# Optimization experiments

Measured on AMD Instinct MI355X. Metric: run time of the kernel, lower is better.

Reference implementation:

```python
import jax, jax.numpy as jnp
import numpy as np
from jax import lax

DN = ('NCHW', 'OIHW', 'NCHW')


def conv3x3(x, w, b):
    y = lax.conv_general_dilated(x, w, (1, 1), [(1, 1), (1, 1)], dimension_numbers=DN)
    return y + b[None, :, None, None]


def lrelu(x, s):
    return jnp.where(x >= 0, x, s * x)


def layernorm_c(x, g, b, eps=1e-5):
    # LayerNorm over embed_dim; tokens are (h,w), so normalize the channel axis
    m = jnp.mean(x, axis=1, keepdims=True)
    v = jnp.var(x, axis=1, keepdims=True)
    return (x - m) / jnp.sqrt(v + eps) * g[None, :, None, None] + b[None, :, None, None]


def bilateral_corr(x1, x2, md):
    # bilateral cost volume on L2-normalized features:
    # out[b,d,h,w] = <x1n[b,:,h-dy,w-dx], x2n[b,:,h+dy,w+dx]>, (dy,dx) in [-md,md]^2
    def l2n(x):
        return x / jnp.maximum(jnp.linalg.norm(x, axis=1, keepdims=True), 1e-12)
    x1n, x2n = l2n(x1), l2n(x2)
    B, C, H, W = x1.shape
    p1 = jnp.pad(x1n, ((0, 0), (0, 0), (md, md), (md, md)))
    p2 = jnp.pad(x2n, ((0, 0), (0, 0), (md, md), (md, md)))
    outs = []
    for dy in range(-md, md + 1):
        for dx in range(-md, md + 1):
            a = p1[:, :, md - dy:md - dy + H, md - dx:md - dx + W]
            b = p2[:, :, md + dy:md + dy + H, md + dx:md + dx + W]
            outs.append(jnp.sum(a * b, axis=1))
    return jnp.stack(outs, axis=1)  # [B, (2md+1)^2, H, W]


def tail(xt, bi, gln, bln, w0, b0, wr1, br1, wr2, br2, w2, b2, w3, b3, wdec, bdec, wf, bf):
    xt = layernorm_c(xt, gln, bln)
    y = conv3x3(jnp.concatenate([xt, bi], axis=1), w0, b0)
    # resblock(64,64): lrelu(conv2(lrelu(conv1(y))) + y), slope 0.1
    s = y
    r = lrelu(conv3x3(y, wr1, br1), 0.1)
    r = conv3x3(r, wr2, br2) + s
    y = lrelu(r, 0.1)
    y = lrelu(conv3x3(y, w2, b2), 0.2)
    y = lrelu(conv3x3(y, w3, b3), 0.2)
    # ConvTranspose2d(64,64,3,stride=2,pad=1,out_pad=1): lhs-dilated conv with flipped kernel
    wd = jnp.transpose(jnp.flip(wdec, (-2, -1)), (1, 0, 2, 3))  # torch [in,out,kh,kw] -> OIHW
    y = lax.conv_general_dilated(y, wd, (1, 1), [(1, 2), (1, 2)], lhs_dilation=(2, 2), dimension_numbers=DN) + bdec[None, :, None, None]
    flow = conv3x3(y, wf, bf)  # [B, 2, 2H, 2W]
    B, _, H2, W2 = flow.shape
    # F.interpolate(scale_factor=4, mode='bilinear', align_corners=False) * 4
    return jax.image.resize(flow, (B, 2, 4 * H2, 4 * W2), method='bilinear') * 4.0


def setup_inputs():
    key = jax.random.key(0)
    ks = jax.random.split(key, 16)
    B, C, H, W = 4, 256, 96, 160
    md = 3
    r = lambda k, s, sc=0.05: jax.random.normal(k, s, jnp.float32) * sc
    return {
        'x1': jax.random.normal(ks[0], (B, C, H, W), jnp.float32),
        'x2': jax.random.normal(ks[1], (B, C, H, W), jnp.float32),
        'xt': jax.random.normal(ks[2], (B, C, H, W), jnp.float32),
        'gln': jnp.ones((C,), jnp.float32),
        'bln': jnp.zeros((C,), jnp.float32),
        'w0': r(ks[3], (64, C + (2 * md + 1) ** 2, 3, 3)),
        'b0': jnp.zeros((64,), jnp.float32),
        'wr1': r(ks[4], (64, 64, 3, 3)), 'br1': jnp.zeros((64,), jnp.float32),
        'wr2': r(ks[5], (64, 64, 3, 3)), 'br2': jnp.zeros((64,), jnp.float32),
        'w2': r(ks[6], (64, 64, 3, 3)), 'b2': jnp.zeros((64,), jnp.float32),
        'w3': r(ks[7], (64, 64, 3, 3)), 'b3': jnp.zeros((64,), jnp.float32),
        'wdec': r(ks[8], (64, 64, 3, 3)), 'bdec': jnp.zeros((64,), jnp.float32),
        'wf': r(ks[9], (2, 64, 3, 3)), 'bf': jnp.zeros((2,), jnp.float32),
        'corr_range': 3,
    }


def reference(x1, x2, xt, gln, bln, w0, b0, wr1, br1, wr2, br2, w2, b2, w3, b3, wdec, bdec, wf, bf, corr_range):
    bi = bilateral_corr(x1, x2, int(corr_range))
    return tail(xt, bi, gln, bln, w0, b0, wr1, br1, wr2, br2, w2, b2, w3, b3, wdec, bdec, wf, bf)
```

## Files before the change

kernel.cpp:

```cpp
#include <hip/hip_runtime.h>
#include <math.h>

#define HH_ 96
#define WW_ 160
#define HW 15360
#define NPIX 61440
#define CC 256
#define C0 320
#define FF 64
#define H2 192
#define W2 320
#define OHW 61440
#define HO 768
#define WO 1280

typedef __attribute__((ext_vector_type(8))) short short8;
typedef __attribute__((ext_vector_type(4))) float f32x4;

__device__ __forceinline__ float bf2f(ushort u) {
    union { unsigned int i; float f; } v; v.i = ((unsigned int)u) << 16; return v.f;
}
__device__ __forceinline__ ushort f2bf(float f) {
    union { float f; unsigned int i; } v; v.f = f;
    unsigned int u = v.i;
    return (ushort)((u + 0x7FFFu + ((u >> 16) & 1u)) >> 16);
}

__global__ __launch_bounds__(256) void normpack_kernel(
    const float* __restrict__ x1, const float* __restrict__ x2, const float* __restrict__ xt,
    const float* __restrict__ gam, const float* __restrict__ bet,
    ushort* __restrict__ x1c, ushort* __restrict__ x2c,
    ushort* __restrict__ Xhi, float* __restrict__ inv1, float* __restrict__ inv2) {
    __shared__ ushort tile[32 * 258];
    __shared__ float sred[4][32][2];
    const int t = threadIdx.x;
    const int w = t >> 6, l = t & 63;
    const int px4 = l & 7;
    const int cbase = t >> 3;
    const int pxt = blockIdx.x, which = blockIdx.y, b = blockIdx.z;
    const float* src = (which == 0 ? x1 : which == 1 ? x2 : xt);
    src += (size_t)b * CC * HW + pxt * 32;

    float s1[4] = {0.f, 0.f, 0.f, 0.f}, s2[4] = {0.f, 0.f, 0.f, 0.f};
#pragma unroll
    for (int it = 0; it < 8; ++it) {
        int c = it * 32 + cbase;
        f32x4 v4 = *(const f32x4*)(src + (size_t)c * HW + px4 * 4);
#pragma unroll
        for (int j = 0; j < 4; ++j) {
            float f = v4[j];
            s1[j] += f; s2[j] += f * f;
            tile[(px4 * 4 + j) * 258 + c] = f2bf(f);
        }
    }
#pragma unroll
    for (int j = 0; j < 4; ++j) {
        s1[j] += __shfl_xor(s1[j], 8);  s1[j] += __shfl_xor(s1[j], 16); s1[j] += __shfl_xor(s1[j], 32);
        s2[j] += __shfl_xor(s2[j], 8);  s2[j] += __shfl_xor(s2[j], 16); s2[j] += __shfl_xor(s2[j], 32);
    }
    if ((l >> 3) == 0) {
#pragma unroll
        for (int j = 0; j < 4; ++j) {
            sred[w][px4 * 4 + j][0] = s1[j];
            sred[w][px4 * 4 + j][1] = s2[j];
        }
    }
    __syncthreads();

    const int px = t >> 3, grp = t & 7;
    float S1 = sred[0][px][0] + sred[1][px][0] + sred[2][px][0] + sred[3][px][0];
    float S2 = sred[0][px][1] + sred[1][px][1] + sred[2][px][1] + sred[3][px][1];
    const int p = b * HW + pxt * 32 + px;
    const ushort* row = &tile[px * 258];
    if (which < 2) {
        float inv = 1.f / fmaxf(sqrtf(S2), 1e-12f);
        if (grp == 0) (which == 0 ? inv1 : inv2)[p] = inv;
        ushort* dst = (which == 0 ? x1c : x2c) + (size_t)p * CC + grp * 32;
#pragma unroll
        for (int k = 0; k < 4; ++k) {
            short8 o;
#pragma unroll
            for (int h = 0; h < 4; ++h) {
                unsigned int u2 = *(const unsigned int*)(row + grp * 32 + k * 8 + h * 2);
                o[h * 2]     = (short)(u2 & 0xFFFF);
                o[h * 2 + 1] = (short)(u2 >> 16);
            }
            *(short8*)(dst + k * 8) = o;
        }
    } else {
        float m = S1 * (1.f / 256.f);
        float var = fmaxf(S2 * (1.f / 256.f) - m * m, 0.f);
        float rs = rsqrtf(var + 1e-5f);
        ushort* dst = Xhi + (size_t)p * C0 + grp * 32;
#pragma unroll
        for (int k = 0; k < 4; ++k) {
            short8 o;
#pragma unroll
            for (int h = 0; h < 4; ++h) {
                unsigned int u2 = *(const unsigned int*)(row + grp * 32 + k * 8 + h * 2);
                int c = grp * 32 + k * 8 + h * 2;
                float f0 = (bf2f((ushort)(u2 & 0xFFFF)) - m) * rs * gam[c] + bet[c];
                float f1 = (bf2f((ushort)(u2 >> 16)) - m) * rs * gam[c + 1] + bet[c + 1];
                o[h * 2]     = (short)f2bf(f0);
                o[h * 2 + 1] = (short)f2bf(f1);
            }
            *(short8*)(dst + k * 8) = o;
        }
        if (grp < 4) {
            short8 z = {0, 0, 0, 0, 0, 0, 0, 0};
            *(short8*)(Xhi + (size_t)p * C0 + 256 + grp * 16) = z;
            *(short8*)(Xhi + (size_t)p * C0 + 256 + grp * 16 + 8) = z;
        }
    }
}

__global__ __launch_bounds__(256) void corr_mfma_kernel(
    const ushort* __restrict__ x1c, const ushort* __restrict__ x2c,
    const float* __restrict__ inv1, const float* __restrict__ inv2,
    ushort* __restrict__ Xhi) {
    const int lane = threadIdx.x & 63;
    const int wv = threadIdx.x >> 6;
    const int sid = ((blockIdx.x & 7) * 120) + (blockIdx.x >> 3);
    const int b  = sid / 240;
    const int rem = sid % 240;
    const int uq = rem / 10, xt = rem % 10;
    const int u = uq * 4 + wv;
    const int x0 = xt * 16;
    const int jl = lane & 15;
    const int kg = lane >> 4;
    const short8 zero8 = {0, 0, 0, 0, 0, 0, 0, 0};

    short8 qf[8];
    {
        size_t qb = ((size_t)b * HW + u * WW_ + x0 + jl) * CC + kg * 8;
#pragma unroll
        for (int ks = 0; ks < 8; ++ks)
            qf[ks] = *(const short8*)(x1c + qb + ks * 32);
    }
    float iv1v[4];
#pragma unroll
    for (int r = 0; r < 4; ++r)
        iv1v[r] = inv1[b * HW + u * WW_ + x0 + kg * 4 + r];

    for (int dy = -3; dy <= 3; ++dy) {
        const int y = u + dy;
        if ((unsigned)y >= (unsigned)HH_) continue;
        const int w = u + 2 * dy;
        const bool rowok = (unsigned)w < (unsigned)HH_;

        f32x4 acc0 = (f32x4){0.f, 0.f, 0.f, 0.f};
        f32x4 acc1 = (f32x4){0.f, 0.f, 0.f, 0.f};
        if (rowok) {
#pragma unroll
            for (int nt = 0; nt < 2; ++nt) {
                int kx = x0 - 6 + jl + 16 * nt;
                bool ok = (unsigned)kx < (unsigned)WW_;
                int kxc = min(max(kx, 0), WW_ - 1);
                size_t kb = ((size_t)b * HW + w * WW_ + kxc) * CC + kg * 8;
#pragma unroll
                for (int ks = 0; ks < 8; ++ks) {
                    short8 bv = *(const short8*)(x2c + kb + ks * 32);
                    if (!ok) bv = zero8;
                    if (nt == 0)
                        acc0 = __builtin_amdgcn_mfma_f32_16x16x32_bf16(qf[ks], bv, acc0, 0, 0, 0);
                    else
                        acc1 = __builtin_amdgcn_mfma_f32_16x16x32_bf16(qf[ks], bv, acc1, 0, 0, 0);
                }
            }
        }
#pragma unroll
        for (int nt = 0; nt < 2; ++nt) {
            int j = jl + 16 * nt;
#pragma unroll
            for (int r = 0; r < 4; ++r) {
                int q = kg * 4 + r;
                int tt = j - q - 6;
                if (tt & 1) continue;
                int dx = tt >> 1;
                if (dx < -3 || dx > 3) continue;
                int cx = x0 + q + dx;
                if ((unsigned)cx >= (unsigned)WW_) continue;
                float v = 0.f;
                if (rowok) {
                    int pbx = min(max(x0 + q + 2 * dx, 0), WW_ - 1);
                    float iv2 = inv2[b * HW + w * WW_ + pbx];
                    v = (nt == 0 ? acc0[r] : acc1[r]) * iv1v[r] * iv2;
                }
                size_t o = ((size_t)(b * HW + y * WW_ + cx)) * C0
                         + 256 + (dy + 3) * 7 + (dx + 3);
                Xhi[o] = f2bf(v);
            }
        }
    }
}

__global__ void pack_w_all(const float* __restrict__ w0, const float* __restrict__ wr1,
                           const float* __restrict__ wr2, const float* __restrict__ w2,
                           const float* __restrict__ w3, const float* __restrict__ wdec,
                           ushort* __restrict__ W0, ushort* __restrict__ WR1,
                           ushort* __restrict__ WR2, ushort* __restrict__ W2o,
                           ushort* __restrict__ W3o, ushort* __restrict__ WD) {
    int job = blockIdx.y;
    const float* w = job == 0 ? w0 : job == 1 ? wr1 : job == 2 ? wr2
                   : job == 3 ? w2 : job == 4 ? w3 : wdec;
    ushort* dst = job == 0 ? W0 : job == 1 ? WR1 : job == 2 ? WR2
                : job == 3 ? W2o : job == 4 ? W3o : WD;
    int CinReal = job == 0 ? 305 : 64;
    int KC = job == 0 ? 10 : 2;
    int isDeconv = (job == 5);
    int gid = blockIdx.x * blockDim.x + threadIdx.x;
    int total = 9 * KC * 4 * 64;
    if (gid >= total) return;
    int lane = gid & 63;
    int nt = (gid >> 6) & 3;
    int kc = (gid >> 8) % KC;
    int slot = (gid >> 8) / KC;
    int co = nt * 16 + (lane & 15);
    int ky = slot / 3, kx = slot % 3;
    for (int j = 0; j < 8; ++j) {
        int ci = kc * 32 + (lane >> 4) * 8 + j;
        float v = 0.f;
        if (ci < CinReal) {
            if (isDeconv) v = w[((size_t)(ci * 64 + co) * 3 + (2 - ky)) * 3 + (2 - kx)];
            else          v = w[((size_t)(co * CinReal + ci) * 3 + ky) * 3 + kx];
        }
        dst[(size_t)gid * 8 + j] = f2bf(v);
    }
}

template<int KC>
__global__ __launch_bounds__(256, 8) void conv_ldsK(
    const ushort* __restrict__ Ahi,
    const ushort* __restrict__ Whi,
    const float* __restrict__ bias,
    ushort* __restrict__ Ohi,
    const ushort* __restrict__ Rhi,
    float slope, int act, int hasres) {
    constexpr int CIN = KC * 32;
    __shared__ ushort lds[2 * 2336];
    const int t = threadIdx.x;
    const int lane = t & 63;
    const int wave = t >> 6;
    const int row_w = wave >> 1;
    const int coh = wave & 1;
    const int kg = lane >> 4;
    const int jl = lane & 15;
    const short8 zero8 = {0, 0, 0, 0, 0, 0, 0, 0};

    const int sid = ((blockIdx.x & 7) * 240) + (blockIdx.x >> 3);
    const int b0 = sid / 480;
    const int rm = sid % 480;
    const int yp = rm / 10, xw = rm % 10;
    const int y0 = yp * 2;
    const int x0 = xw * 16;
    const size_t rowbase = (size_t)b0 * HW;

    f32x4 acc[2];
    acc[0] = (f32x4){0.f, 0.f, 0.f, 0.f};
    acc[1] = (f32x4){0.f, 0.f, 0.f, 0.f};

    auto stage = [&](ushort* buf, int kc) {
#pragma unroll
        for (int i = 0; i < 2; ++i) {
            int e = t + i * 256;
            if (e < 288) {
                int kge = e & 3;
                int q = e >> 2;
                int pe = q % 18;
                int re = q / 18;
                int gy = y0 - 1 + re, gx = x0 - 1 + pe;
                bool ok = ((unsigned)gy < 96u) && ((unsigned)gx < 160u);
                short8 vh = zero8;
                if (ok) {
                    size_t ga = ((rowbase + gy * WW_ + gx) * (size_t)CIN) + kc * 32 + kge * 8;
                    vh = *(const short8*)(Ahi + ga);
                }
                *(short8*)(buf + kge * 584 + (re * 18 + pe) * 8) = vh;
            }
        }
    };

    stage(lds, 0);

#pragma unroll 1
    for (int kc = 0; kc < KC; ++kc) {
        __syncthreads();
        if (kc + 1 < KC) stage(lds + ((kc + 1) & 1) * 2336, kc + 1);
        const ushort* bufc = lds + (kc & 1) * 2336;
#pragma unroll
        for (int tap = 0; tap < 9; ++tap) {
            const int dy = tap / 3 - 1, dx = tap % 3 - 1;
            const int abase = kg * 584 + (row_w + dy + 1) * 144 + (jl + dx + 1) * 8;
            short8 ah = *(const short8*)(bufc + abase);
            const ushort* wt = Whi + (size_t)(tap * KC + kc) * 2048;
#pragma unroll
            for (int nt = 0; nt < 2; ++nt) {
                short8 bh = *(const short8*)(wt + (((coh << 1) | nt) * 64 + lane) * 8);
                acc[nt] = __builtin_amdgcn_mfma_f32_16x16x32_bf16(ah, bh, acc[nt], 0, 0, 0);
            }
        }
    }

#pragma unroll
    for (int r = 0; r < 4; ++r) {
        size_t pr = rowbase + (y0 + row_w) * WW_ + x0 + kg * 4 + r;
#pragma unroll
        for (int nt = 0; nt < 2; ++nt) {
            int co = ((coh << 1) | nt) * 16 + jl;
            float vv = acc[nt][r] + bias[co];
            size_t oo = pr * 64 + co;
            if (hasres) vv += bf2f(Rhi[oo]);
            if (act) vv = vv >= 0.f ? vv : vv * slope;
            Ohi[oo] = f2bf(vv);
        }
    }
}

__global__ __launch_bounds__(256, 6) void deconv_fused_kernel(
    const ushort* __restrict__ Ahi,
    const ushort* __restrict__ Whi,
    const float* __restrict__ bias,
    ushort* __restrict__ decb) {
    const int lane = threadIdx.x & 63;
    const int wave = threadIdx.x >> 6;
    const int row_w = wave >> 1;
    const int coh = wave & 1;
    const int kg = lane >> 4;
    const short8 zero8 = {0, 0, 0, 0, 0, 0, 0, 0};

    const int sid = ((blockIdx.x & 7) * 240) + (blockIdx.x >> 3);
    const int b0 = sid / 480;
    const int rm = sid % 480;
    const int yp = rm / 10, xh = rm % 10;
    const int y0 = yp * 2 + row_w;
    const int x0 = xh * 16;
    const size_t rowbase = (size_t)b0 * HW;

    f32x4 acc[4][2];
#pragma unroll
    for (int p = 0; p < 4; ++p) {
        acc[p][0] = (f32x4){0.f, 0.f, 0.f, 0.f};
        acc[p][1] = (f32x4){0.f, 0.f, 0.f, 0.f};
    }

    const int nuse[4]   = {4, 2, 2, 1};
    const int upar[4][4] = {{0, 1, 2, 3}, {1, 3, -1, -1}, {2, 3, -1, -1}, {3, -1, -1, -1}};
    const int uslt[4][4] = {{4, 3, 1, 0}, {5, 2, -1, -1}, {7, 6, -1, -1}, {8, -1, -1, -1}};

#pragma unroll
    for (int o = 0; o < 4; ++o) {
        const int ody = o >> 1, odx = o & 1;
        int yy = y0 + ody, xx = x0 + (lane & 15) + odx;
        bool v = (unsigned)yy < 96u && (unsigned)xx < 160u;
        int yyc = min(yy, 95), xxc = min(xx, 159);
        size_t a = (rowbase + yyc * WW_ + xxc) * 64 + kg * 8;
#pragma unroll
        for (int kc = 0; kc < 2; ++kc) {
            short8 ah = *(const short8*)(Ahi + a + kc * 32);
            if (!v) ah = zero8;
#pragma unroll
            for (int u = 0; u < 4; ++u) {
                if (u >= nuse[o]) break;
                int par = upar[o][u], slot = uslt[o][u];
#pragma unroll
                for (int nt = 0; nt < 2; ++nt) {
                    short8 bh = *(const short8*)(Whi + ((size_t)slot * 2 + kc) * 2048
                                                 + (((coh << 1) | nt) * 64 + lane) * 8);
                    acc[par][nt] = __builtin_amdgcn_mfma_f32_16x16x32_bf16(ah, bh, acc[par][nt], 0, 0, 0);
                }
            }
        }
    }

#pragma unroll
    for (int r = 0; r < 4; ++r) {
        int x2 = x0 + kg * 4 + r;
#pragma unroll
        for (int par = 0; par < 4; ++par) {
            int py = par >> 1, px = par & 1;
            size_t po = ((size_t)b0 * H2 + 2 * y0 + py) * W2 + 2 * x2 + px;
#pragma unroll
            for (int nt = 0; nt < 2; ++nt) {
                int co = ((coh << 1) | nt) * 16 + (lane & 15);
                decb[po * 64 + co] = f2bf(acc[par][nt][r] + bias[co]);
            }
        }
    }
}

__global__ __launch_bounds__(256) void flow_kernel(const ushort* __restrict__ decb,
                                                   const float* __restrict__ wf,
                                                   const float* __restrict__ bf2v,
                                                   float* __restrict__ flow) {
    __shared__ float wsm[1152];
    for (int i = threadIdx.x; i < 1152; i += 256) wsm[i] = wf[i];
    __syncthreads();
    int fid = ((blockIdx.x & 7) * 240) + (blockIdx.x >> 3);
    int tid = fid * 256 + threadIdx.x;
    int p = tid >> 1, half = tid & 1;
    if (p >= 4 * OHW) return;
    int b = p / OHW, rem = p % OHW, oy = rem / W2, ox = rem % W2;
    float a0 = 0.f, a1 = 0.f;
    for (int ky = 0; ky < 3; ++ky) {
        int yy = oy + ky - 1;
        if ((unsigned)yy >= (unsigned)H2) continue;
        for (int kx = 0; kx < 3; ++kx) {
            int xx = ox + kx - 1;
            if ((unsigned)xx >= (unsigned)W2) continue;
            size_t base = ((size_t)b * OHW + yy * W2 + xx) * 64;
            int tap = ky * 3 + kx;
#pragma unroll
            for (int c8 = 0; c8 < 4; ++c8) {
                int cg = half * 4 + c8;
                short8 v8 = *(const short8*)(decb + base + cg * 8);
#pragma unroll
                for (int j = 0; j < 8; ++j) {
                    float f = bf2f((ushort)v8[j]);
                    int ci = cg * 8 + j;
                    a0 += f * wsm[ci * 9 + tap];
                    a1 += f * wsm[(64 + ci) * 9 + tap];
                }
            }
        }
    }
    a0 += __shfl_xor(a0, 1);
    a1 += __shfl_xor(a1, 1);
    if (half == 0) {
        flow[(size_t)(b * 2 + 0) * OHW + rem] = a0 + bf2v[0];
        flow[(size_t)(b * 2 + 1) * OHW + rem] = a1 + bf2v[1];
    }
}

__global__ __launch_bounds__(256) void resize_kernel(const float* __restrict__ flow,
                                                     float* __restrict__ out) {
    int idx = blockIdx.x * blockDim.x + threadIdx.x;
    int total = 4 * 2 * HO * (WO / 4);
    if (idx >= total) return;
    int qx = idx % (WO / 4);
    int oy = (idx / (WO / 4)) % HO;
    int c  = (idx / ((WO / 4) * HO)) % 2;
    int b  = idx / ((WO / 4) * HO * 2);

    float sy = (oy + 0.5f) * 0.25f - 0.5f;
    int y0 = (int)floorf(sy);
    float fy = sy - y0;
    int y0c = min(max(y0, 0), H2 - 1);
    int y1c = min(max(y0 + 1, 0), H2 - 1);
    const float* r0 = flow + ((size_t)(b * 2 + c) * H2 + y0c) * W2;
    const float* r1 = flow + ((size_t)(b * 2 + c) * H2 + y1c) * W2;
    int xm = max(qx - 1, 0), xp = min(qx + 1, W2 - 1);
    float fm = (1.f - fy) * r0[xm] + fy * r1[xm];
    float f0 = (1.f - fy) * r0[qx] + fy * r1[qx];
    float fp = (1.f - fy) * r0[xp] + fy * r1[xp];
    f32x4 o;
    o[0] = (0.375f * fm + 0.625f * f0) * 4.0f;
    o[1] = (0.125f * fm + 0.875f * f0) * 4.0f;
    o[2] = (0.875f * f0 + 0.125f * fp) * 4.0f;
    o[3] = (0.625f * f0 + 0.375f * fp) * 4.0f;
    *(f32x4*)(out + (((size_t)(b * 2 + c) * HO + oy) * WO) + qx * 4) = o;
}

extern "C" void kernel_launch(void* const* d_in, const int* in_sizes, int n_in,
                              void* d_out, int out_size, void* d_ws, size_t ws_size,
                              hipStream_t stream) {
    const float* x1   = (const float*)d_in[0];
    const float* x2   = (const float*)d_in[1];
    const float* xt   = (const float*)d_in[2];
    const float* gln  = (const float*)d_in[3];
    const float* bln  = (const float*)d_in[4];
    const float* w0   = (const float*)d_in[5];
    const float* b0   = (const float*)d_in[6];
    const float* wr1  = (const float*)d_in[7];
    const float* br1  = (const float*)d_in[8];
    const float* wr2  = (const float*)d_in[9];
    const float* br2  = (const float*)d_in[10];
    const float* w2   = (const float*)d_in[11];
    const float* b2   = (const float*)d_in[12];
    const float* w3   = (const float*)d_in[13];
    const float* b3   = (const float*)d_in[14];
    const float* wdec = (const float*)d_in[15];
    const float* bdec = (const float*)d_in[16];
    const float* wf   = (const float*)d_in[17];
    const float* bfv  = (const float*)d_in[18];
    float* out = (float*)d_out;

    char* ws = (char*)d_ws;
    ushort* x1c  = (ushort*)(ws + 0);
    ushort* x2c  = (ushort*)(ws + 31457280);
    ushort* X0hi = (ushort*)(ws + 62914560);
    ushort* y0hi = (ushort*)(ws + 102236160);
    ushort* t1hi = (ushort*)(ws + 110100480);
    ushort* t2hi = (ushort*)(ws + 117964800);
    ushort* decb = (ushort*)(ws + 0);
    float*  flowb = (float*)(ws + 62914560);
    char* wp = ws + 125829120;
    ushort* W0hi  = (ushort*)(wp);
    ushort* WR1hi = (ushort*)(wp + 368640);
    ushort* WR2hi = (ushort*)(wp + 442368);
    ushort* W2hi  = (ushort*)(wp + 516096);
    ushort* W3hi  = (ushort*)(wp + 589824);
    ushort* WDhi  = (ushort*)(wp + 663552);
    float*  inv1  = (float*)(wp + 786432);
    float*  inv2  = (float*)(wp + 1048576);

    pack_w_all<<<dim3(90, 6), 256, 0, stream>>>(w0, wr1, wr2, w2, w3, wdec,
        W0hi, WR1hi, WR2hi, W2hi, W3hi, WDhi);

    normpack_kernel<<<dim3(480, 3, 4), 256, 0, stream>>>(
        x1, x2, xt, gln, bln, x1c, x2c, X0hi, inv1, inv2);
    corr_mfma_kernel<<<960, 256, 0, stream>>>(x1c, x2c, inv1, inv2, X0hi);

    conv_ldsK<10><<<1920, 256, 0, stream>>>(X0hi, W0hi, b0, y0hi, nullptr, 0.f, 0, 0);
    conv_ldsK<2><<<1920, 256, 0, stream>>>(y0hi, WR1hi, br1, t1hi, nullptr, 0.1f, 1, 0);
    conv_ldsK<2><<<1920, 256, 0, stream>>>(t1hi, WR2hi, br2, t2hi, y0hi, 0.1f, 1, 1);
    conv_ldsK<2><<<1920, 256, 0, stream>>>(t2hi, W2hi, b2, t1hi, nullptr, 0.2f, 1, 0);
    conv_ldsK<2><<<1920, 256, 0, stream>>>(t1hi, W3hi, b3, t2hi, nullptr, 0.2f, 1, 0);
    deconv_fused_kernel<<<1920, 256, 0, stream>>>(t2hi, WDhi, bdec, decb);

    flow_kernel<<<1920, 256, 0, stream>>>(decb, wf, bfv, flowb);
    resize_kernel<<<7680, 256, 0, stream>>>(flowb, out);

    (void)in_sizes; (void)n_in; (void)out_size; (void)ws_size;
}
```

Measured before the change: 348.0 us.

## Enlarge conv tiles to 8 rows per block with two rows per wave

The 3x3 conv kernel now handles an 8-row by 16-column output tile per 512-thread block instead of 2 rows per 256-thread block. Each wave computes two output rows and reuses every loaded weight fragment across two MFMAs. This is meant to cut halo overhead in the LDS staging and halve weight loads per MFMA. In exchange it uses more LDS and registers per block and launches only 480 blocks, which lowers occupancy and parallelism on the GPU.

```diff
diff --git a/kernel.cpp b/kernel.cpp
--- a/kernel.cpp
+++ b/kernel.cpp
@@ -229,7 +229,7 @@
 }
 
 template<int KC>
-__global__ __launch_bounds__(256, 8) void conv_ldsK(
+__global__ __launch_bounds__(512) void conv_big(
     const ushort* __restrict__ Ahi,
     const ushort* __restrict__ Whi,
     const float* __restrict__ bias,
@@ -237,33 +237,36 @@
     const ushort* __restrict__ Rhi,
     float slope, int act, int hasres) {
     constexpr int CIN = KC * 32;
-    __shared__ ushort lds[2 * 2336];
+    __shared__ ushort lds[2 * 5920];
     const int t = threadIdx.x;
     const int lane = t & 63;
     const int wave = t >> 6;
-    const int row_w = wave >> 1;
+    const int rp = wave >> 1;
     const int coh = wave & 1;
     const int kg = lane >> 4;
     const int jl = lane & 15;
     const short8 zero8 = {0, 0, 0, 0, 0, 0, 0, 0};
 
-    const int sid = ((blockIdx.x & 7) * 240) + (blockIdx.x >> 3);
-    const int b0 = sid / 480;
-    const int rm = sid % 480;
-    const int yp = rm / 10, xw = rm % 10;
-    const int y0 = yp * 2;
+    const int sid = ((blockIdx.x & 7) * 60) + (blockIdx.x >> 3);
+    const int b0 = sid / 120;
+    const int rm = sid % 120;
+    const int yo = rm / 10, xw = rm % 10;
+    const int y0 = yo * 8;
     const int x0 = xw * 16;
     const size_t rowbase = (size_t)b0 * HW;
 
-    f32x4 acc[2];
-    acc[0] = (f32x4){0.f, 0.f, 0.f, 0.f};
-    acc[1] = (f32x4){0.f, 0.f, 0.f, 0.f};
+    f32x4 acc[2][2];
+#pragma unroll
+    for (int r = 0; r < 2; ++r) {
+        acc[r][0] = (f32x4){0.f, 0.f, 0.f, 0.f};
+        acc[r][1] = (f32x4){0.f, 0.f, 0.f, 0.f};
+    }
 
     auto stage = [&](ushort* buf, int kc) {
 #pragma unroll
         for (int i = 0; i < 2; ++i) {
-            int e = t + i * 256;
-            if (e < 288) {
+            int e = t + i * 512;
+            if (e < 720) {
                 int kge = e & 3;
                 int q = e >> 2;
                 int pe = q % 18;
@@ -275,7 +278,7 @@
                     size_t ga = ((rowbase + gy * WW_ + gx) * (size_t)CIN) + kc * 32 + kge * 8;
                     vh = *(const short8*)(Ahi + ga);
                 }
-                *(short8*)(buf + kge * 584 + (re * 18 + pe) * 8) = vh;
+                *(short8*)(buf + kge * 1480 + (re * 18 + pe) * 8) = vh;
             }
         }
     };
@@ -285,33 +288,39 @@
 #pragma unroll 1
     for (int kc = 0; kc < KC; ++kc) {
         __syncthreads();
-        if (kc + 1 < KC) stage(lds + ((kc + 1) & 1) * 2336, kc + 1);
-        const ushort* bufc = lds + (kc & 1) * 2336;
+        if (kc + 1 < KC) stage(lds + ((kc + 1) & 1) * 5920, kc + 1);
+        const ushort* bufc = lds + (kc & 1) * 5920;
 #pragma unroll
         for (int tap = 0; tap < 9; ++tap) {
             const int dy = tap / 3 - 1, dx = tap % 3 - 1;
-            const int abase = kg * 584 + (row_w + dy + 1) * 144 + (jl + dx + 1) * 8;
-            short8 ah = *(const short8*)(bufc + abase);
+            const int a0i = kg * 1480 + ((rp * 2 + 0 + dy + 1) * 18 + (jl + dx + 1)) * 8;
+            const int a1i = kg * 1480 + ((rp * 2 + 1 + dy + 1) * 18 + (jl + dx + 1)) * 8;
+            short8 ah0 = *(const short8*)(bufc + a0i);
+            short8 ah1 = *(const short8*)(bufc + a1i);
             const ushort* wt = Whi + (size_t)(tap * KC + kc) * 2048;
 #pragma unroll
             for (int nt = 0; nt < 2; ++nt) {
                 short8 bh = *(const short8*)(wt + (((coh << 1) | nt) * 64 + lane) * 8);
-                acc[nt] = __builtin_amdgcn_mfma_f32_16x16x32_bf16(ah, bh, acc[nt], 0, 0, 0);
-            }
-        }
-    }
-
-#pragma unroll
-    for (int r = 0; r < 4; ++r) {
-        size_t pr = rowbase + (y0 + row_w) * WW_ + x0 + kg * 4 + r;
-#pragma unroll
-        for (int nt = 0; nt < 2; ++nt) {
-            int co = ((coh << 1) | nt) * 16 + jl;
-            float vv = acc[nt][r] + bias[co];
-            size_t oo = pr * 64 + co;
-            if (hasres) vv += bf2f(Rhi[oo]);
-            if (act) vv = vv >= 0.f ? vv : vv * slope;
-            Ohi[oo] = f2bf(vv);
+                acc[0][nt] = __builtin_amdgcn_mfma_f32_16x16x32_bf16(ah0, bh, acc[0][nt], 0, 0, 0);
+                acc[1][nt] = __builtin_amdgcn_mfma_f32_16x16x32_bf16(ah1, bh, acc[1][nt], 0, 0, 0);
+            }
+        }
+    }
+
+#pragma unroll
+    for (int rr = 0; rr < 2; ++rr) {
+#pragma unroll
+        for (int r = 0; r < 4; ++r) {
+            size_t pr = rowbase + (y0 + rp * 2 + rr) * WW_ + x0 + kg * 4 + r;
+#pragma unroll
+            for (int nt = 0; nt < 2; ++nt) {
+                int co = ((coh << 1) | nt) * 16 + jl;
+                float vv = acc[rr][nt][r] + bias[co];
+                size_t oo = pr * 64 + co;
+                if (hasres) vv += bf2f(Rhi[oo]);
+                if (act) vv = vv >= 0.f ? vv : vv * slope;
+                Ohi[oo] = f2bf(vv);
+            }
         }
     }
 }
@@ -510,11 +519,11 @@
         x1, x2, xt, gln, bln, x1c, x2c, X0hi, inv1, inv2);
     corr_mfma_kernel<<<960, 256, 0, stream>>>(x1c, x2c, inv1, inv2, X0hi);
 
-    conv_ldsK<10><<<1920, 256, 0, stream>>>(X0hi, W0hi, b0, y0hi, nullptr, 0.f, 0, 0);
-    conv_ldsK<2><<<1920, 256, 0, stream>>>(y0hi, WR1hi, br1, t1hi, nullptr, 0.1f, 1, 0);
-    conv_ldsK<2><<<1920, 256, 0, stream>>>(t1hi, WR2hi, br2, t2hi, y0hi, 0.1f, 1, 1);
-    conv_ldsK<2><<<1920, 256, 0, stream>>>(t2hi, W2hi, b2, t1hi, nullptr, 0.2f, 1, 0);
-    conv_ldsK<2><<<1920, 256, 0, stream>>>(t1hi, W3hi, b3, t2hi, nullptr, 0.2f, 1, 0);
+    conv_big<10><<<480, 512, 0, stream>>>(X0hi, W0hi, b0, y0hi, nullptr, 0.f, 0, 0);
+    conv_big<2><<<480, 512, 0, stream>>>(y0hi, WR1hi, br1, t1hi, nullptr, 0.1f, 1, 0);
+    conv_big<2><<<480, 512, 0, stream>>>(t1hi, WR2hi, br2, t2hi, y0hi, 0.1f, 1, 1);
+    conv_big<2><<<480, 512, 0, stream>>>(t2hi, W2hi, b2, t1hi, nullptr, 0.2f, 1, 0);
+    conv_big<2><<<480, 512, 0, stream>>>(t1hi, W3hi, b3, t2hi, nullptr, 0.2f, 1, 0);
     deconv_fused_kernel<<<1920, 256, 0, stream>>>(t2hi, WDhi, bdec, decb);
 
     flow_kernel<<<1920, 256, 0, stream>>>(decb, wf, bfv, flowb);
```

Result: faster. 333.7 us (-4.1%).
